# Optimization experiments

Measured on AMD Instinct MI355X. Metric: run time of the kernel, lower is better.

Reference implementation:

```python
import jax, jax.numpy as jnp
import numpy as np

B, T, D, H = 16, 2048, 1024, 64  # batch, seq_len(block_sz), emb_dim, head_sz


def setup_inputs() -> dict:
    key = jax.random.key(0)
    k0, k1, k2, k3 = jax.random.split(key, 4)
    x = jax.random.normal(k0, (B, T, D), dtype=jnp.float32)
    # nn.Linear(D, H, bias=False) weights, stored as [D, H] so y = x @ W
    s = 1.0 / np.sqrt(D)
    Wq = jax.random.uniform(k1, (D, H), dtype=jnp.float32, minval=-s, maxval=s)
    Wk = jax.random.uniform(k2, (D, H), dtype=jnp.float32, minval=-s, maxval=s)
    Wv = jax.random.uniform(k3, (D, H), dtype=jnp.float32, minval=-s, maxval=s)
    return {"x": x, "Wq": Wq, "Wk": Wk, "Wv": Wv}


def reference(x, Wq, Wk, Wv):
    # Single-head causal self-attention, naive (materializes full [B,T,T] scores).
    q = x @ Wq  # [B, T, H]
    k = x @ Wk  # [B, T, H]
    v = x @ Wv  # [B, T, H]
    scale = 1.0 / (q.shape[-1] ** 0.5)
    w = jnp.einsum("btd,bsd->bts", q, k) * scale  # [B, T, T]
    causal = jnp.tril(jnp.ones((T, T), dtype=bool))
    w = jnp.where(causal, w, -jnp.inf)
    w = jax.nn.softmax(w, axis=-1)
    # dropout p=0.0 -> identity
    out = jnp.einsum("bts,bsd->btd", w, v)  # [B, T, H]
    return out
```

## Files before the change

kernel.cpp:

```cpp
#include <hip/hip_runtime.h>
#include <hip/hip_bf16.h>
#include <math.h>

#define BB 16
#define TT 2048
#define DD 1024
#define HH 64
#define QK_SCALE 0.18033688011112042f

typedef short bf16x8 __attribute__((ext_vector_type(8)));
typedef short bf16x4 __attribute__((ext_vector_type(4)));
typedef float f32x4 __attribute__((ext_vector_type(4)));

__device__ __forceinline__ short f2bf(float f) {
  union { float f; unsigned u; } c; c.f = f;
  unsigned u = c.u + 0x7FFFu + ((c.u >> 16) & 1u);
  return (short)(u >> 16);
}

__device__ __forceinline__ unsigned pk2(float lo, float hi) {
  float2 t; t.x = lo; t.y = hi;
  __hip_bfloat162 h = __float22bfloat162_rn(t);
  union { __hip_bfloat162 h; unsigned u; } c; c.h = h;
  return c.u;
}

__device__ __forceinline__ void* lds_swz(void* base, int row, int col) {
  int byte = (row << 7) + (col << 1);
  byte ^= (row & 7) << 4;
  return (void*)((char*)base + byte);
}

__device__ __forceinline__ void pack16(const float4& a0, const float4& a1,
                                       const float4& a2, const float4& a3,
                                       bf16x8& s0, bf16x8& s1) {
  unsigned* u0 = (unsigned*)&s0;
  unsigned* u1 = (unsigned*)&s1;
  u0[0] = pk2(a0.x, a0.y); u0[1] = pk2(a0.z, a0.w);
  u0[2] = pk2(a1.x, a1.y); u0[3] = pk2(a1.z, a1.w);
  u1[0] = pk2(a2.x, a2.y); u1[1] = pk2(a2.z, a2.w);
  u1[2] = pk2(a3.x, a3.y); u1[3] = pk2(a3.z, a3.w);
}

__global__ __launch_bounds__(256) void pack_wt(
    const float* __restrict__ Wq, const float* __restrict__ Wk,
    const float* __restrict__ Wv, short* __restrict__ wt) {
  const int idx = blockIdx.x * 256 + threadIdx.x;
  const int n = idx >> 7;
  const int k0 = (idx & 127) << 3;
  const float* W = (n < 64) ? Wq : (n < 128) ? Wk : Wv;
  const int h = n & 63;
  bf16x8 o;
#pragma unroll
  for (int j = 0; j < 8; ++j) o[j] = f2bf(W[(k0 + j) * HH + h]);
  *(bf16x8*)&wt[n * DD + k0] = o;
}

__global__ __launch_bounds__(256) void qkv_mfma(
    const float* __restrict__ x, const short* __restrict__ wt,
    short* __restrict__ qo, short* __restrict__ ko, short* __restrict__ vt) {
  __shared__ short xs[2][64 * 64];
  const int tid = threadIdx.x;
  const int lane = tid & 63;
  const int w = tid >> 6;
  const int q16 = lane & 15;
  const int g = lane >> 4;
  const size_t r0 = (size_t)blockIdx.x * 64;

  const int srow = tid >> 2;
  const int sc = (tid & 3) << 4;
  const float* xrow = x + (r0 + srow) * DD + sc;

  f32x4 acc[4][3];
#pragma unroll
  for (int mf = 0; mf < 4; ++mf)
#pragma unroll
    for (int nf = 0; nf < 3; ++nf) acc[mf][nf] = (f32x4){0.f, 0.f, 0.f, 0.f};

  const short* wp[3];
#pragma unroll
  for (int nf = 0; nf < 3; ++nf)
    wp[nf] = wt + (size_t)(w * 48 + nf * 16 + q16) * DD + g * 8;

  float4 xa[2][4];
  {
    const float4* xp = (const float4*)xrow;
#pragma unroll
    for (int j = 0; j < 4; ++j) xa[0][j] = xp[j];
    bf16x8 s0, s1;
    pack16(xa[0][0], xa[0][1], xa[0][2], xa[0][3], s0, s1);
    *(bf16x8*)lds_swz(xs[0], srow, sc) = s0;
    *(bf16x8*)lds_swz(xs[0], srow, sc + 8) = s1;
    const float4* xp1 = (const float4*)(xrow + 64);
#pragma unroll
    for (int j = 0; j < 4; ++j) xa[1][j] = xp1[j];
  }
  bf16x8 bcur[3][2];
#pragma unroll
  for (int nf = 0; nf < 3; ++nf)
#pragma unroll
    for (int kf = 0; kf < 2; ++kf)
      bcur[nf][kf] = *(const bf16x8*)(wp[nf] + kf * 32);
  __syncthreads();

  int cur = 0;
#pragma unroll 2
  for (int ks = 0; ks < 16; ++ks) {
    const int pnext = (ks + 1) & 1;
    const int pfree = ks & 1;
    if (ks < 14) {
      const float4* xp = (const float4*)(xrow + (ks + 2) * 64);
#pragma unroll
      for (int j = 0; j < 4; ++j) xa[pfree][j] = xp[j];
    }
    bf16x8 bnxt[3][2];
    if (ks < 15) {
      const int k1 = (ks + 1) << 6;
#pragma unroll
      for (int nf = 0; nf < 3; ++nf)
#pragma unroll
        for (int kf = 0; kf < 2; ++kf)
          bnxt[nf][kf] = *(const bf16x8*)(wp[nf] + k1 + kf * 32);
    }

    bf16x8 afr[4][2];
#pragma unroll
    for (int mf = 0; mf < 4; ++mf)
#pragma unroll
      for (int kf = 0; kf < 2; ++kf)
        afr[mf][kf] = *(bf16x8*)lds_swz(xs[cur], mf * 16 + q16, kf * 32 + g * 8);

#pragma unroll
    for (int mf = 0; mf < 4; ++mf)
#pragma unroll
      for (int nf = 0; nf < 3; ++nf)
#pragma unroll
        for (int kf = 0; kf < 2; ++kf)
          acc[mf][nf] = __builtin_amdgcn_mfma_f32_16x16x32_bf16(
              afr[mf][kf], bcur[nf][kf], acc[mf][nf], 0, 0, 0);

    if (ks < 15) {
      bf16x8 s0, s1;
      pack16(xa[pnext][0], xa[pnext][1], xa[pnext][2], xa[pnext][3], s0, s1);
      *(bf16x8*)lds_swz(xs[cur ^ 1], srow, sc) = s0;
      *(bf16x8*)lds_swz(xs[cur ^ 1], srow, sc + 8) = s1;
      __syncthreads();
      cur ^= 1;
#pragma unroll
      for (int nf = 0; nf < 3; ++nf)
#pragma unroll
        for (int kf = 0; kf < 2; ++kf) bcur[nf][kf] = bnxt[nf][kf];
    }
  }

#pragma unroll
  for (int nf = 0; nf < 3; ++nf) {
    const int n = w * 48 + nf * 16 + q16;
    const int mat = n >> 6;
    const int h = n & 63;
    if (mat < 2) {
      short* outp = mat ? ko : qo;
      const float fac = mat ? 1.0f : QK_SCALE;
#pragma unroll
      for (int mf = 0; mf < 4; ++mf)
#pragma unroll
        for (int r = 0; r < 4; ++r)
          outp[(r0 + mf * 16 + g * 4 + r) * HH + h] = f2bf(acc[mf][nf][r] * fac);
    } else {
      const int bb = (int)(r0 >> 11);
      const int tloc = (int)(r0 & 2047);
#pragma unroll
      for (int mf = 0; mf < 4; ++mf) {
        uint2 pkv;
        pkv.x = pk2(acc[mf][nf][0], acc[mf][nf][1]);
        pkv.y = pk2(acc[mf][nf][2], acc[mf][nf][3]);
        *(uint2*)&vt[((size_t)bb * HH + h) * TT + tloc + mf * 16 + g * 4] = pkv;
      }
    }
  }
}

__global__ __launch_bounds__(256, 4) void attn_mfma(
    const short* __restrict__ q, const short* __restrict__ k,
    const short* __restrict__ vt, float* __restrict__ out) {
  __shared__ short klds[2][64 * 64];
  __shared__ short vlds[2][64 * 64];

  const int id = blockIdx.x;
  const int b = (id & 7) | (((id >> 3) & 1) << 3);
  const int kk = id >> 4;
  const int qt = (kk < 16) ? (31 - kk) : (kk - 16);
  const int t0 = qt << 6;
  const int tid = threadIdx.x;
  const int lane = tid & 63;
  const int w = tid >> 6;
  const int q16 = lane & 15;
  const int g = lane >> 4;
  const int NC = qt + 1;

  const size_t brow = (size_t)b * TT;
  const short* kg = k + brow * HH;
  const short* vtg = vt + (size_t)b * HH * TT;

  const int srow = tid >> 2;
  const int scol = (tid & 3) << 4;

  const int vgA = (scol >> 3) & 3;
  const int vgB = ((scol + 8) >> 3) & 3;
  const int vm2 = scol >> 5;
  const short* vrow_p = vtg + srow * TT + vm2 * 32;

  bf16x8 kr0 = *(const bf16x8*)&kg[srow * HH + scol];
  bf16x8 kr1 = *(const bf16x8*)&kg[srow * HH + scol + 8];
  bf16x4 va0 = *(const bf16x4*)(vrow_p + 4 * vgA);
  bf16x4 va1 = *(const bf16x4*)(vrow_p + 16 + 4 * vgA);
  bf16x4 vb0 = *(const bf16x4*)(vrow_p + 4 * vgB);
  bf16x4 vb1 = *(const bf16x4*)(vrow_p + 16 + 4 * vgB);

  {
    const short* qsrc = q + (brow + t0 + srow) * HH;
    *(bf16x8*)lds_swz(klds[0], srow, scol) = *(const bf16x8*)&qsrc[scol];
    *(bf16x8*)lds_swz(klds[0], srow, scol + 8) = *(const bf16x8*)&qsrc[scol + 8];
  }
  __syncthreads();
  bf16x8 qa[2];
#pragma unroll
  for (int kf = 0; kf < 2; ++kf)
    qa[kf] = *(bf16x8*)lds_swz(klds[0], w * 16 + q16, kf * 32 + g * 8);
  __syncthreads();

  *(bf16x8*)lds_swz(klds[0], srow, scol) = kr0;
  *(bf16x8*)lds_swz(klds[0], srow, scol + 8) = kr1;
  *(bf16x8*)lds_swz(vlds[0], srow, scol) =
      __builtin_shufflevector(va0, va1, 0, 1, 2, 3, 4, 5, 6, 7);
  *(bf16x8*)lds_swz(vlds[0], srow, scol + 8) =
      __builtin_shufflevector(vb0, vb1, 0, 1, 2, 3, 4, 5, 6, 7);
  __syncthreads();

  f32x4 po[4];
  f32x4 lacc = (f32x4){0.f, 0.f, 0.f, 0.f};
  float m = -INFINITY;
#pragma unroll
  for (int nf = 0; nf < 4; ++nf) po[nf] = (f32x4){0.f, 0.f, 0.f, 0.f};

  const bf16x8 ones = {0x3F80, 0x3F80, 0x3F80, 0x3F80,
                       0x3F80, 0x3F80, 0x3F80, 0x3F80};
  int cur = 0;

  for (int c = 0; c < NC; ++c) {
    const bool notlast = (c + 1 < NC);
    if (notlast) {
      const int s1 = (c + 1) << 6;
      kr0 = *(const bf16x8*)&kg[(s1 + srow) * HH + scol];
      kr1 = *(const bf16x8*)&kg[(s1 + srow) * HH + scol + 8];
      va0 = *(const bf16x4*)(vrow_p + s1 + 4 * vgA);
      va1 = *(const bf16x4*)(vrow_p + s1 + 16 + 4 * vgA);
      vb0 = *(const bf16x4*)(vrow_p + s1 + 4 * vgB);
      vb1 = *(const bf16x4*)(vrow_p + s1 + 16 + 4 * vgB);
    }

    f32x4 sfr[4];
#pragma unroll
    for (int nf = 0; nf < 4; ++nf) sfr[nf] = (f32x4){0.f, 0.f, 0.f, 0.f};
    __builtin_amdgcn_s_setprio(1);
#pragma unroll
    for (int nf = 0; nf < 4; ++nf)
#pragma unroll
      for (int kf = 0; kf < 2; ++kf) {
        bf16x8 kb = *(bf16x8*)lds_swz(klds[cur], nf * 16 + q16, kf * 32 + g * 8);
        sfr[nf] = __builtin_amdgcn_mfma_f32_16x16x32_bf16(kb, qa[kf], sfr[nf], 0, 0, 0);
      }
    __builtin_amdgcn_s_setprio(0);

    if (c == NC - 1) {
      const int qloc = w * 16 + q16;
#pragma unroll
      for (int nf = 0; nf < 4; ++nf)
#pragma unroll
        for (int r = 0; r < 4; ++r)
          if (16 * nf + 4 * g + r > qloc) sfr[nf][r] = -INFINITY;
    }

    float pm;
    {
      f32x4 t01 = (f32x4){fmaxf(sfr[0][0], sfr[1][0]), fmaxf(sfr[0][1], sfr[1][1]),
                          fmaxf(sfr[0][2], sfr[1][2]), fmaxf(sfr[0][3], sfr[1][3])};
      f32x4 t23 = (f32x4){fmaxf(sfr[2][0], sfr[3][0]), fmaxf(sfr[2][1], sfr[3][1]),
                          fmaxf(sfr[2][2], sfr[3][2]), fmaxf(sfr[2][3], sfr[3][3])};
      pm = fmaxf(fmaxf(fmaxf(t01[0], t23[0]), fmaxf(t01[1], t23[1])),
                 fmaxf(fmaxf(t01[2], t23[2]), fmaxf(t01[3], t23[3])));
      pm = fmaxf(pm, __shfl_xor(pm, 16));
      pm = fmaxf(pm, __shfl_xor(pm, 32));
    }

    if (__any(pm - m > 8.f)) {
      const float mn = fmaxf(m, pm);
      const float corr = exp2f(m - mn);
      m = mn;
      const int sbase = (lane & 48) + ((lane >> 4) << 2);
#pragma unroll
      for (int r = 0; r < 4; ++r) {
        const float cr = __shfl(corr, sbase + r);
        lacc[r] *= cr;
#pragma unroll
        for (int nf = 0; nf < 4; ++nf) po[nf][r] *= cr;
      }
    }

    bf16x8 pa[2];
#pragma unroll
    for (int m2 = 0; m2 < 2; ++m2) {
      float e0 = exp2f(sfr[2 * m2][0] - m), e1 = exp2f(sfr[2 * m2][1] - m);
      float e2 = exp2f(sfr[2 * m2][2] - m), e3 = exp2f(sfr[2 * m2][3] - m);
      float e4 = exp2f(sfr[2 * m2 + 1][0] - m), e5 = exp2f(sfr[2 * m2 + 1][1] - m);
      float e6 = exp2f(sfr[2 * m2 + 1][2] - m), e7 = exp2f(sfr[2 * m2 + 1][3] - m);
      unsigned* up = (unsigned*)&pa[m2];
      up[0] = pk2(e0, e1); up[1] = pk2(e2, e3);
      up[2] = pk2(e4, e5); up[3] = pk2(e6, e7);
    }

    __builtin_amdgcn_s_setprio(1);
#pragma unroll
    for (int m2 = 0; m2 < 2; ++m2) {
#pragma unroll
      for (int nf = 0; nf < 4; ++nf) {
        bf16x8 vb = *(bf16x8*)lds_swz(vlds[cur], nf * 16 + q16, m2 * 32 + g * 8);
        po[nf] = __builtin_amdgcn_mfma_f32_16x16x32_bf16(pa[m2], vb, po[nf], 0, 0, 0);
      }
      lacc = __builtin_amdgcn_mfma_f32_16x16x32_bf16(pa[m2], ones, lacc, 0, 0, 0);
    }
    __builtin_amdgcn_s_setprio(0);

    if (notlast) {
      *(bf16x8*)lds_swz(klds[cur ^ 1], srow, scol) = kr0;
      *(bf16x8*)lds_swz(klds[cur ^ 1], srow, scol + 8) = kr1;
      *(bf16x8*)lds_swz(vlds[cur ^ 1], srow, scol) =
          __builtin_shufflevector(va0, va1, 0, 1, 2, 3, 4, 5, 6, 7);
      *(bf16x8*)lds_swz(vlds[cur ^ 1], srow, scol + 8) =
          __builtin_shufflevector(vb0, vb1, 0, 1, 2, 3, 4, 5, 6, 7);
      __syncthreads();
      cur ^= 1;
    }
  }

  const int qrow = t0 + w * 16 + g * 4;
#pragma unroll
  for (int nf = 0; nf < 4; ++nf) {
    const int h = nf * 16 + q16;
#pragma unroll
    for (int r = 0; r < 4; ++r)
      out[(brow + qrow + r) * HH + h] = po[nf][r] / lacc[r];
  }
}

extern "C" void kernel_launch(void* const* d_in, const int* in_sizes, int n_in,
                              void* d_out, int out_size, void* d_ws, size_t ws_size,
                              hipStream_t stream) {
  const float* x  = (const float*)d_in[0];
  const float* Wq = (const float*)d_in[1];
  const float* Wk = (const float*)d_in[2];
  const float* Wv = (const float*)d_in[3];
  float* out = (float*)d_out;

  const size_t bth = (size_t)BB * TT * HH;
  short* qb  = (short*)d_ws;
  short* kb  = qb + bth;
  short* vtb = kb + bth;
  short* wtb = vtb + bth;

  pack_wt<<<96, 256, 0, stream>>>(Wq, Wk, Wv, wtb);
  qkv_mfma<<<(BB * TT) / 64, 256, 0, stream>>>(x, wtb, qb, kb, vtb);
  attn_mfma<<<512, 256, 0, stream>>>(qb, kb, vtb, out);
}
```

Baseline: 80.97 us.

## Widen QKV projection K-step to 128 and drop register prefetch of weights

The QKV projection kernel now stages 128 columns of x per iteration (8 steps instead of 16), halving the barrier count, and uses a wider swizzled LDS layout. The weight fragments are no longer double-buffered in registers but loaded per kf sub-step inside the loop. The x prefetch goes from two buffers to one, and launch bounds request 3 blocks per CU so register use is capped. The aim is lower sync overhead and register pressure with higher occupancy, at the cost of less latency hiding for the weight loads.

```diff
diff --git a/kernel.cpp b/kernel.cpp
--- a/kernel.cpp
+++ b/kernel.cpp
@@ -30,16 +30,10 @@
   byte ^= (row & 7) << 4;
   return (void*)((char*)base + byte);
 }
-
-__device__ __forceinline__ void pack16(const float4& a0, const float4& a1,
-                                       const float4& a2, const float4& a3,
-                                       bf16x8& s0, bf16x8& s1) {
-  unsigned* u0 = (unsigned*)&s0;
-  unsigned* u1 = (unsigned*)&s1;
-  u0[0] = pk2(a0.x, a0.y); u0[1] = pk2(a0.z, a0.w);
-  u0[2] = pk2(a1.x, a1.y); u0[3] = pk2(a1.z, a1.w);
-  u1[0] = pk2(a2.x, a2.y); u1[1] = pk2(a2.z, a2.w);
-  u1[2] = pk2(a3.x, a3.y); u1[3] = pk2(a3.z, a3.w);
+__device__ __forceinline__ void* lds_swz256(void* base, int row, int col) {
+  int byte = (row << 8) + (col << 1);
+  byte ^= (row & 7) << 4;
+  return (void*)((char*)base + byte);
 }
 
 __global__ __launch_bounds__(256) void pack_wt(
@@ -56,10 +50,10 @@
   *(bf16x8*)&wt[n * DD + k0] = o;
 }
 
-__global__ __launch_bounds__(256) void qkv_mfma(
+__global__ __launch_bounds__(256, 3) void qkv_mfma(
     const float* __restrict__ x, const short* __restrict__ wt,
     short* __restrict__ qo, short* __restrict__ ko, short* __restrict__ vt) {
-  __shared__ short xs[2][64 * 64];
+  __shared__ short xs[2][64 * 128];
   const int tid = threadIdx.x;
   const int lane = tid & 63;
   const int w = tid >> 6;
@@ -68,8 +62,8 @@
   const size_t r0 = (size_t)blockIdx.x * 64;
 
   const int srow = tid >> 2;
-  const int sc = (tid & 3) << 4;
-  const float* xrow = x + (r0 + srow) * DD + sc;
+  const int sce = (tid & 3) << 5;
+  const float* xrow = x + (r0 + srow) * DD + sce;
 
   f32x4 acc[4][3];
 #pragma unroll
@@ -82,74 +76,63 @@
   for (int nf = 0; nf < 3; ++nf)
     wp[nf] = wt + (size_t)(w * 48 + nf * 16 + q16) * DD + g * 8;
 
-  float4 xa[2][4];
+  float4 xa[8];
   {
     const float4* xp = (const float4*)xrow;
 #pragma unroll
-    for (int j = 0; j < 4; ++j) xa[0][j] = xp[j];
-    bf16x8 s0, s1;
-    pack16(xa[0][0], xa[0][1], xa[0][2], xa[0][3], s0, s1);
-    *(bf16x8*)lds_swz(xs[0], srow, sc) = s0;
-    *(bf16x8*)lds_swz(xs[0], srow, sc + 8) = s1;
-    const float4* xp1 = (const float4*)(xrow + 64);
-#pragma unroll
-    for (int j = 0; j < 4; ++j) xa[1][j] = xp1[j];
-  }
-  bf16x8 bcur[3][2];
-#pragma unroll
-  for (int nf = 0; nf < 3; ++nf)
-#pragma unroll
-    for (int kf = 0; kf < 2; ++kf)
-      bcur[nf][kf] = *(const bf16x8*)(wp[nf] + kf * 32);
+    for (int j = 0; j < 8; ++j) xa[j] = xp[j];
+#pragma unroll
+    for (int u = 0; u < 4; ++u) {
+      bf16x8 s;
+      unsigned* up = (unsigned*)&s;
+      up[0] = pk2(xa[2 * u].x, xa[2 * u].y);
+      up[1] = pk2(xa[2 * u].z, xa[2 * u].w);
+      up[2] = pk2(xa[2 * u + 1].x, xa[2 * u + 1].y);
+      up[3] = pk2(xa[2 * u + 1].z, xa[2 * u + 1].w);
+      *(bf16x8*)lds_swz256(xs[0], srow, sce + u * 8) = s;
+    }
+  }
   __syncthreads();
 
   int cur = 0;
-#pragma unroll 2
-  for (int ks = 0; ks < 16; ++ks) {
-    const int pnext = (ks + 1) & 1;
-    const int pfree = ks & 1;
-    if (ks < 14) {
-      const float4* xp = (const float4*)(xrow + (ks + 2) * 64);
-#pragma unroll
-      for (int j = 0; j < 4; ++j) xa[pfree][j] = xp[j];
-    }
-    bf16x8 bnxt[3][2];
-    if (ks < 15) {
-      const int k1 = (ks + 1) << 6;
+  for (int ks = 0; ks < 8; ++ks) {
+    if (ks < 7) {
+      const float4* xp = (const float4*)(xrow + (ks + 1) * 128);
+#pragma unroll
+      for (int j = 0; j < 8; ++j) xa[j] = xp[j];
+    }
+
+#pragma unroll
+    for (int kf = 0; kf < 4; ++kf) {
+      bf16x8 bw[3];
 #pragma unroll
       for (int nf = 0; nf < 3; ++nf)
-#pragma unroll
-        for (int kf = 0; kf < 2; ++kf)
-          bnxt[nf][kf] = *(const bf16x8*)(wp[nf] + k1 + kf * 32);
-    }
-
-    bf16x8 afr[4][2];
-#pragma unroll
-    for (int mf = 0; mf < 4; ++mf)
-#pragma unroll
-      for (int kf = 0; kf < 2; ++kf)
-        afr[mf][kf] = *(bf16x8*)lds_swz(xs[cur], mf * 16 + q16, kf * 32 + g * 8);
-
-#pragma unroll
-    for (int mf = 0; mf < 4; ++mf)
-#pragma unroll
-      for (int nf = 0; nf < 3; ++nf)
-#pragma unroll
-        for (int kf = 0; kf < 2; ++kf)
+        bw[nf] = *(const bf16x8*)(wp[nf] + ks * 128 + kf * 32);
+      bf16x8 af[4];
+#pragma unroll
+      for (int mf = 0; mf < 4; ++mf)
+        af[mf] = *(bf16x8*)lds_swz256(xs[cur], mf * 16 + q16, kf * 32 + g * 8);
+#pragma unroll
+      for (int mf = 0; mf < 4; ++mf)
+#pragma unroll
+        for (int nf = 0; nf < 3; ++nf)
           acc[mf][nf] = __builtin_amdgcn_mfma_f32_16x16x32_bf16(
-              afr[mf][kf], bcur[nf][kf], acc[mf][nf], 0, 0, 0);
-
-    if (ks < 15) {
-      bf16x8 s0, s1;
-      pack16(xa[pnext][0], xa[pnext][1], xa[pnext][2], xa[pnext][3], s0, s1);
-      *(bf16x8*)lds_swz(xs[cur ^ 1], srow, sc) = s0;
-      *(bf16x8*)lds_swz(xs[cur ^ 1], srow, sc + 8) = s1;
+              af[mf], bw[nf], acc[mf][nf], 0, 0, 0);
+    }
+
+    if (ks < 7) {
+#pragma unroll
+      for (int u = 0; u < 4; ++u) {
+        bf16x8 s;
+        unsigned* up = (unsigned*)&s;
+        up[0] = pk2(xa[2 * u].x, xa[2 * u].y);
+        up[1] = pk2(xa[2 * u].z, xa[2 * u].w);
+        up[2] = pk2(xa[2 * u + 1].x, xa[2 * u + 1].y);
+        up[3] = pk2(xa[2 * u + 1].z, xa[2 * u + 1].w);
+        *(bf16x8*)lds_swz256(xs[cur ^ 1], srow, sce + u * 8) = s;
+      }
       __syncthreads();
       cur ^= 1;
-#pragma unroll
-      for (int nf = 0; nf < 3; ++nf)
-#pragma unroll
-        for (int kf = 0; kf < 2; ++kf) bcur[nf][kf] = bnxt[nf][kf];
     }
   }
 
```

After: 90.99 us. 12.4% more time.

## Stream x tiles into LDS via direct global-to-LDS loads with triple buffering

Applied to the files above, without the earlier changes.

Replaces the register-staged x loading in the QKV projection (global load, convert to bf16, store to LDS) with direct global_load_lds transfers of fp32 data into a swizzled triple-buffered LDS ring. The bf16 conversion moves to the LDS read side, and explicit vmcnt waits plus barriers replace __syncthreads. The aim is to cut VGPR pressure and instruction overhead in the load path so more loads stay in flight, with launch bounds requesting two blocks per CU. In exchange, LDS use grows to 48KB of fp32 per block and conversion work is repeated for each fragment read.

```diff
diff --git a/kernel.cpp b/kernel.cpp
--- a/kernel.cpp
+++ b/kernel.cpp
@@ -25,21 +25,21 @@
   return c.u;
 }
 
+__device__ __forceinline__ void fence_vm4_barrier() {
+  asm volatile("s_waitcnt vmcnt(4)" ::: "memory");
+  __builtin_amdgcn_sched_barrier(0);
+  __builtin_amdgcn_s_barrier();
+}
+__device__ __forceinline__ void fence_vm0_barrier() {
+  asm volatile("s_waitcnt vmcnt(0)" ::: "memory");
+  __builtin_amdgcn_sched_barrier(0);
+  __builtin_amdgcn_s_barrier();
+}
+
 __device__ __forceinline__ void* lds_swz(void* base, int row, int col) {
   int byte = (row << 7) + (col << 1);
   byte ^= (row & 7) << 4;
   return (void*)((char*)base + byte);
-}
-
-__device__ __forceinline__ void pack16(const float4& a0, const float4& a1,
-                                       const float4& a2, const float4& a3,
-                                       bf16x8& s0, bf16x8& s1) {
-  unsigned* u0 = (unsigned*)&s0;
-  unsigned* u1 = (unsigned*)&s1;
-  u0[0] = pk2(a0.x, a0.y); u0[1] = pk2(a0.z, a0.w);
-  u0[2] = pk2(a1.x, a1.y); u0[3] = pk2(a1.z, a1.w);
-  u1[0] = pk2(a2.x, a2.y); u1[1] = pk2(a2.z, a2.w);
-  u1[2] = pk2(a3.x, a3.y); u1[3] = pk2(a3.z, a3.w);
 }
 
 __global__ __launch_bounds__(256) void pack_wt(
@@ -56,10 +56,10 @@
   *(bf16x8*)&wt[n * DD + k0] = o;
 }
 
-__global__ __launch_bounds__(256) void qkv_mfma(
+__global__ __launch_bounds__(256, 2) void qkv_mfma(
     const float* __restrict__ x, const short* __restrict__ wt,
     short* __restrict__ qo, short* __restrict__ ko, short* __restrict__ vt) {
-  __shared__ short xs[2][64 * 64];
+  __shared__ float xls[3][64 * 64];
   const int tid = threadIdx.x;
   const int lane = tid & 63;
   const int w = tid >> 6;
@@ -67,10 +67,6 @@
   const int g = lane >> 4;
   const size_t r0 = (size_t)blockIdx.x * 64;
 
-  const int srow = tid >> 2;
-  const int sc = (tid & 3) << 4;
-  const float* xrow = x + (r0 + srow) * DD + sc;
-
   f32x4 acc[4][3];
 #pragma unroll
   for (int mf = 0; mf < 4; ++mf)
@@ -82,37 +78,33 @@
   for (int nf = 0; nf < 3; ++nf)
     wp[nf] = wt + (size_t)(w * 48 + nf * 16 + q16) * DD + g * 8;
 
-  float4 xa[2][4];
-  {
-    const float4* xp = (const float4*)xrow;
-#pragma unroll
-    for (int j = 0; j < 4; ++j) xa[0][j] = xp[j];
-    bf16x8 s0, s1;
-    pack16(xa[0][0], xa[0][1], xa[0][2], xa[0][3], s0, s1);
-    *(bf16x8*)lds_swz(xs[0], srow, sc) = s0;
-    *(bf16x8*)lds_swz(xs[0], srow, sc + 8) = s1;
-    const float4* xp1 = (const float4*)(xrow + 64);
-#pragma unroll
-    for (int j = 0; j < 4; ++j) xa[1][j] = xp1[j];
-  }
+  const int srow_b = w * 16 + (lane >> 4);
+  const int ul = lane & 15;
+
   bf16x8 bcur[3][2];
 #pragma unroll
   for (int nf = 0; nf < 3; ++nf)
 #pragma unroll
     for (int kf = 0; kf < 2; ++kf)
       bcur[nf][kf] = *(const bf16x8*)(wp[nf] + kf * 32);
-  __syncthreads();
-
-  int cur = 0;
-#pragma unroll 2
+#pragma unroll
+  for (int t = 0; t < 2; ++t)
+#pragma unroll
+    for (int j = 0; j < 4; ++j) {
+      const int row = srow_b + j * 4;
+      const int us = ul ^ (row & 7);
+      const float* src = x + (r0 + row) * DD + t * 64 + us * 4;
+      __builtin_amdgcn_global_load_lds(
+          (const __attribute__((address_space(1))) void*)src,
+          (__attribute__((address_space(3))) void*)(&xls[t][0] + (w * 4 + j) * 256),
+          16, 0, 0);
+    }
+  __builtin_amdgcn_sched_barrier(0);
+  fence_vm4_barrier();
+
   for (int ks = 0; ks < 16; ++ks) {
-    const int pnext = (ks + 1) & 1;
-    const int pfree = ks & 1;
-    if (ks < 14) {
-      const float4* xp = (const float4*)(xrow + (ks + 2) * 64);
-#pragma unroll
-      for (int j = 0; j < 4; ++j) xa[pfree][j] = xp[j];
-    }
+    const float* bufc = &xls[ks % 3][0];
+
     bf16x8 bnxt[3][2];
     if (ks < 15) {
       const int k1 = (ks + 1) << 6;
@@ -122,13 +114,37 @@
         for (int kf = 0; kf < 2; ++kf)
           bnxt[nf][kf] = *(const bf16x8*)(wp[nf] + k1 + kf * 32);
     }
+    if (ks < 14) {
+#pragma unroll
+      for (int j = 0; j < 4; ++j) {
+        const int row = srow_b + j * 4;
+        const int us = ul ^ (row & 7);
+        const float* src = x + (r0 + row) * DD + (ks + 2) * 64 + us * 4;
+        __builtin_amdgcn_global_load_lds(
+            (const __attribute__((address_space(1))) void*)src,
+            (__attribute__((address_space(3))) void*)(&xls[(ks + 2) % 3][0] +
+                                                      (w * 4 + j) * 256),
+            16, 0, 0);
+      }
+    }
+    __builtin_amdgcn_sched_barrier(0);
 
     bf16x8 afr[4][2];
 #pragma unroll
     for (int mf = 0; mf < 4; ++mf)
 #pragma unroll
-      for (int kf = 0; kf < 2; ++kf)
-        afr[mf][kf] = *(bf16x8*)lds_swz(xs[cur], mf * 16 + q16, kf * 32 + g * 8);
+      for (int kf = 0; kf < 2; ++kf) {
+        const int R = mf * 16 + q16;
+        const int r7 = R & 7;
+        const int u0 = kf * 8 + g * 2;
+        const float4 fa = *(const float4*)(bufc + R * 64 + ((u0 ^ r7) << 2));
+        const float4 fb = *(const float4*)(bufc + R * 64 + (((u0 + 1) ^ r7) << 2));
+        unsigned* up = (unsigned*)&afr[mf][kf];
+        up[0] = pk2(fa.x, fa.y);
+        up[1] = pk2(fa.z, fa.w);
+        up[2] = pk2(fb.x, fb.y);
+        up[3] = pk2(fb.z, fb.w);
+      }
 
 #pragma unroll
     for (int mf = 0; mf < 4; ++mf)
@@ -140,12 +156,7 @@
               afr[mf][kf], bcur[nf][kf], acc[mf][nf], 0, 0, 0);
 
     if (ks < 15) {
-      bf16x8 s0, s1;
-      pack16(xa[pnext][0], xa[pnext][1], xa[pnext][2], xa[pnext][3], s0, s1);
-      *(bf16x8*)lds_swz(xs[cur ^ 1], srow, sc) = s0;
-      *(bf16x8*)lds_swz(xs[cur ^ 1], srow, sc + 8) = s1;
-      __syncthreads();
-      cur ^= 1;
+      if (ks < 14) fence_vm4_barrier(); else fence_vm0_barrier();
 #pragma unroll
       for (int nf = 0; nf < 3; ++nf)
 #pragma unroll
```

Measured after the change: 79.06 us. 2.4% less time.
